# Kernel tuning notes

Measured on AMD Instinct MI355X. Metric: run time of the kernel, lower is better.

Reference implementation:

```python
import jax, jax.numpy as jnp
import numpy as np

H = 8        # heads
DH = 64      # dim_head
EPS = 1e-5   # LayerNorm eps (torch default)


def setup_inputs() -> dict:
    key = jax.random.key(0)
    k0, k1, k2, k3, k4 = jax.random.split(key, 5)
    b, l, n, dim = 2, 8, 256, 512
    inner = H * DH
    return {
        "xyzs": jax.random.normal(k0, (b, l, n, 3), dtype=jnp.float32),
        "features": jax.random.normal(k1, (b, l, n, dim), dtype=jnp.float32),
        "ln_gamma": jnp.ones((dim,), dtype=jnp.float32),
        "ln_beta": jnp.zeros((dim,), dtype=jnp.float32),
        "w_qkv": jax.random.normal(k2, (dim, 3 * inner), dtype=jnp.float32) * 0.02,
        "w_sp": jax.random.normal(k3, (3, DH), dtype=jnp.float32) * 0.3,
        "w_out": jax.random.normal(k4, (inner, dim), dtype=jnp.float32) * 0.02,
        "b_out": jnp.zeros((dim,), dtype=jnp.float32),
    }


def reference(xyzs, features, ln_gamma, ln_beta, w_qkv, w_sp, w_out, b_out):
    b, l, n, dim = features.shape
    m = l * n
    inner = H * DH
    scale = DH ** (-0.5)

    # LayerNorm over last dim (biased variance, eps=1e-5)
    mu = jnp.mean(features, axis=-1, keepdims=True)
    var = jnp.var(features, axis=-1, keepdims=True)
    normed = (features - mu) * jax.lax.rsqrt(var + EPS) * ln_gamma + ln_beta

    # qkv projection, chunk into q,k,v, reshape 'b l n (h d) -> b h (l n) d'
    qkv = normed.reshape(b, m, dim) @ w_qkv            # [b, m, 3*inner]
    def split_heads(t):
        return t.reshape(b, m, H, DH).transpose(0, 2, 1, 3)  # [b, h, m, d]
    q = split_heads(qkv[..., :inner])
    k = split_heads(qkv[..., inner:2 * inner])
    v = split_heads(qkv[..., 2 * inner:])

    dots = jnp.einsum('bhid,bhjd->bhij', q, k) * scale  # [b, h, m, m]
    attn = jax.nn.softmax(dots, axis=-1)
    v_out = jnp.einsum('bhij,bhjd->bhid', attn, v)      # [b, h, m, d]

    # pairwise coordinate deltas: delta[b,i,j,c] = xyz[b,j,c] - xyz[b,i,c]
    xyz_f = xyzs.reshape(b, m, 3)
    delta = xyz_f[:, None, :, :] - xyz_f[:, :, None, :]  # [b, m, m, 3]
    # attention-weighted aggregation over j (avoids [b,h,m,m,3] intermediate)
    agg = jnp.einsum('bhij,bijc->bhic', attn, delta)     # [b, h, m, 3]
    disp = agg @ w_sp                                    # [b, h, m, DH]

    out = v_out + disp                                   # [b, h, m, DH]
    out = out.transpose(0, 2, 1, 3).reshape(b, m, inner) # 'b h m d -> b m (h d)'
    out = jax.nn.gelu(out @ w_out + b_out, approximate=False)
    return out.reshape(b, l, n, dim) + features
```

## Files before the change

kernel.cpp:

```cpp
#include <hip/hip_runtime.h>
#include <hip/hip_bf16.h>
#include <math.h>

#define BB   2
#define MM   2048
#define DIM  512
#define NH   8
#define DHd  64
#define NQK  1536
#define ROWS 4096
#define NROW 32768
#define SPLITK 4

typedef __hip_bfloat16 bf16;
typedef __attribute__((ext_vector_type(8))) short bf16x8;
typedef __attribute__((ext_vector_type(4))) float f32x4;
typedef __attribute__((ext_vector_type(8))) unsigned short us8;

__device__ __forceinline__ unsigned short f2bf_bits(float x) {
    bf16 h = __float2bfloat16(x);
    return *(unsigned short*)&h;
}
__device__ __forceinline__ float bf2f(unsigned short u) {
    unsigned int v = ((unsigned int)u) << 16;
    return __uint_as_float(v);
}

__global__ __launch_bounds__(256) void pre_kernel(
    const float* __restrict__ feat, const float* __restrict__ gamma,
    const float* __restrict__ beta, unsigned short* __restrict__ normed,
    const float* __restrict__ wqkv, const float* __restrict__ wout,
    unsigned short* __restrict__ wqkvT, unsigned short* __restrict__ woutT)
{
    __shared__ float st[64][65];
    int b = blockIdx.x;
    int tid = threadIdx.x;
    if (b < ROWS) {
        const float* fr = feat + (size_t)b * DIM;
        float x0 = fr[tid];
        float x1 = fr[tid + 256];
        float s  = x0 + x1;
        float ss = x0 * x0 + x1 * x1;
        #pragma unroll
        for (int o = 32; o >= 1; o >>= 1) { s += __shfl_down(s, o); ss += __shfl_down(ss, o); }
        __shared__ float ws_[4], wss_[4];
        int wid = tid >> 6, lane = tid & 63;
        if (lane == 0) { ws_[wid] = s; wss_[wid] = ss; }
        __syncthreads();
        if (tid == 0) {
            float a = 0.f, c = 0.f;
            for (int i = 0; i < 4; i++) { a += ws_[i]; c += wss_[i]; }
            ws_[0] = a; wss_[0] = c;
        }
        __syncthreads();
        float mu  = ws_[0] * (1.0f / DIM);
        float var = wss_[0] * (1.0f / DIM) - mu * mu;
        float inv = rsqrtf(var + 1e-5f);
        normed[(size_t)b * DIM + tid]       = f2bf_bits((x0 - mu) * inv * gamma[tid] + beta[tid]);
        normed[(size_t)b * DIM + tid + 256] = f2bf_bits((x1 - mu) * inv * gamma[tid + 256] + beta[tid + 256]);
        return;
    }
    int idx = b - ROWS;
    const float* in; unsigned short* out; int N, n0;
    if (idx < 192) { in = wqkv; out = wqkvT; N = NQK; n0 = (idx >> 3) * 64; }
    else { idx -= 192; in = wout; out = woutT; N = DIM; n0 = (idx >> 3) * 64; }
    int k0 = (idx & 7) * 64;
    #pragma unroll
    for (int p = 0; p < 16; p++) {
        int e = tid + p * 256;
        int r = e >> 6, c = e & 63;
        st[r][c] = in[(size_t)(k0 + r) * N + n0 + c];
    }
    __syncthreads();
    #pragma unroll
    for (int p = 0; p < 16; p++) {
        int e = tid + p * 256;
        int nr = e >> 6, kc = e & 63;
        out[(size_t)(n0 + nr) * DIM + k0 + kc] = f2bf_bits(st[kc][nr]);
    }
}

__global__ __launch_bounds__(256) void qkv_gemm(
    const unsigned short* __restrict__ A, const unsigned short* __restrict__ BT,
    unsigned short* __restrict__ qd, unsigned short* __restrict__ kd,
    unsigned short* __restrict__ vd)
{
    __shared__ __align__(16) unsigned short sA[128 * 40];
    __shared__ __align__(16) unsigned short sB[128 * 40];
    int tid = threadIdx.x;
    int r0 = blockIdx.x * 128;
    int n0 = blockIdx.y * 128;
    int chunk = n0 >> 9;
    int cl    = n0 & 511;
    int w = tid >> 6, lane = tid & 63;
    int wm = w >> 1, wn = w & 1;
    int ln15 = lane & 15, quad = lane >> 4;

    int srow = tid >> 1;
    int scol = (tid & 1) * 16;

    f32x4 acc[4][4] = {};

    for (int k0 = 0; k0 < DIM; k0 += 32) {
        __syncthreads();
        *(us8*)&sA[srow * 40 + scol]     = *(const us8*)&A[(size_t)(r0 + srow) * DIM + k0 + scol];
        *(us8*)&sA[srow * 40 + scol + 8] = *(const us8*)&A[(size_t)(r0 + srow) * DIM + k0 + scol + 8];
        *(us8*)&sB[srow * 40 + scol]     = *(const us8*)&BT[(size_t)(n0 + srow) * DIM + k0 + scol];
        *(us8*)&sB[srow * 40 + scol + 8] = *(const us8*)&BT[(size_t)(n0 + srow) * DIM + k0 + scol + 8];
        __syncthreads();
        const unsigned short* fa = (chunk == 2) ? sA : sB;
        const unsigned short* fb = (chunk == 2) ? sB : sA;
        bf16x8 af[4], bf_[4];
        #pragma unroll
        for (int i = 0; i < 4; i++)
            af[i] = *(const bf16x8*)&fa[(wm * 64 + i * 16 + ln15) * 40 + quad * 8];
        #pragma unroll
        for (int j = 0; j < 4; j++)
            bf_[j] = *(const bf16x8*)&fb[(wn * 64 + j * 16 + ln15) * 40 + quad * 8];
        #pragma unroll
        for (int i = 0; i < 4; i++)
            #pragma unroll
            for (int j = 0; j < 4; j++)
                acc[i][j] = __builtin_amdgcn_mfma_f32_16x16x32_bf16(af[i], bf_[j], acc[i][j], 0, 0, 0);
    }

    if (chunk == 2) {
        int rowb = r0 + wm * 64 + quad * 4;
        #pragma unroll
        for (int j = 0; j < 4; j++) {
            int c = cl + wn * 64 + j * 16 + ln15;
            int h = c >> 6, d = c & 63;
            #pragma unroll
            for (int i = 0; i < 4; i++) {
                int gr = rowb + i * 16;
                int bb = gr >> 11, mm = gr & 2047;
                ushort4 pk;
                pk.x = f2bf_bits(acc[i][j][0]);
                pk.y = f2bf_bits(acc[i][j][1]);
                pk.z = f2bf_bits(acc[i][j][2]);
                pk.w = f2bf_bits(acc[i][j][3]);
                *(ushort4*)&vd[((size_t)(bb * NH + h) * DHd + d) * MM + mm] = pk;
            }
        }
    } else {
        unsigned short* dst = (chunk == 0) ? qd : kd;
        float sc = (chunk == 0) ? 0.125f : 1.0f;
        #pragma unroll
        for (int i = 0; i < 4; i++) {
            int within0 = cl + wm * 64 + i * 16 + quad * 4;
            int h = within0 >> 6, d = within0 & 63;
            #pragma unroll
            for (int j = 0; j < 4; j++) {
                int gr = r0 + wn * 64 + j * 16 + ln15;
                int bb = gr >> 11, mm = gr & 2047;
                ushort4 pk;
                pk.x = f2bf_bits(acc[i][j][0] * sc);
                pk.y = f2bf_bits(acc[i][j][1] * sc);
                pk.z = f2bf_bits(acc[i][j][2] * sc);
                pk.w = f2bf_bits(acc[i][j][3] * sc);
                *(ushort4*)&dst[((size_t)(bb * NH + h) * MM + mm) * DHd + d] = pk;
            }
        }
    }
}

__global__ __launch_bounds__(256, 4) void attn_kernel(
    const unsigned short* __restrict__ qg, const unsigned short* __restrict__ kg,
    const unsigned short* __restrict__ vg, const float* __restrict__ xyzs,
    unsigned short* __restrict__ obuf, float* __restrict__ lbuf)
{
    __shared__ __align__(16) unsigned short sK[64 * 72];
    __shared__ __align__(16) unsigned short sVT[80 * 72];
    __shared__ __align__(16) unsigned short sP[128 * 72];

    int tid = threadIdx.x;
    int bh = blockIdx.y; int bb = bh >> 3;
    int i0 = blockIdx.x * 128;
    int ks = blockIdx.z;
    int w = tid >> 6;
    int lane = tid & 63;
    int ln15 = lane & 15;
    int quad = lane >> 4;

    for (int e = tid; e < 12 * 72; e += 256) sVT[68 * 72 + e] = 0;
    if (tid < 64) sVT[67 * 72 + tid] = 0x3F80;

    bf16x8 aq[2][2];
    {
        const unsigned short* q0 = qg + ((size_t)bh * MM + i0 + w * 32 + ln15) * DHd + quad * 8;
        aq[0][0] = *(const bf16x8*)q0;
        aq[0][1] = *(const bf16x8*)(q0 + 32);
        aq[1][0] = *(const bf16x8*)(q0 + 16 * DHd);
        aq[1][1] = *(const bf16x8*)(q0 + 16 * DHd + 32);
    }

    f32x4 o[2][5] = {};

    const unsigned short* kbase = kg + (size_t)bh * MM * DHd;
    const unsigned short* vbase = vg + (size_t)bh * DHd * MM;
    int jbeg = ks * (MM / SPLITK), jend = jbeg + (MM / SPLITK);

    int srow = tid >> 2, scol16 = (tid & 3) * 16;

    us8 rk0, rk1, rv0, rv1;
    float rx = 0.f;
    {
        const unsigned short* src = kbase + (size_t)jbeg * DHd;
        rk0 = *(const us8*)&src[(size_t)tid * 16];
        rk1 = *(const us8*)&src[(size_t)tid * 16 + 8];
        const unsigned short* vs = vbase + jbeg;
        rv0 = *(const us8*)&vs[(size_t)srow * MM + scol16];
        rv1 = *(const us8*)&vs[(size_t)srow * MM + scol16 + 8];
        if (tid < 192) rx = xyzs[((size_t)bb * MM + jbeg) * 3 + tid];
    }

    int pwb = quad << 4;
    int swzr = (ln15 >> 2) << 4;
    int pr0 = (quad * 8) ^ swzr;
    int pr1 = (32 + quad * 8) ^ swzr;

    for (int jt = jbeg; jt < jend; jt += 64) {
        __syncthreads();
        *(us8*)&sK[srow * 72 + scol16]      = rk0;
        *(us8*)&sK[srow * 72 + scol16 + 8]  = rk1;
        *(us8*)&sVT[srow * 72 + scol16]     = rv0;
        *(us8*)&sVT[srow * 72 + scol16 + 8] = rv1;
        if (tid < 192) {
            int key = tid / 3, c = tid - key * 3;
            sVT[(64 + c) * 72 + key] = f2bf_bits(rx);
        }
        __syncthreads();
        int jn = jt + 64;
        if (jn < jend) {
            const unsigned short* src = kbase + (size_t)jn * DHd;
            rk0 = *(const us8*)&src[(size_t)tid * 16];
            rk1 = *(const us8*)&src[(size_t)tid * 16 + 8];
            const unsigned short* vs = vbase + jn;
            rv0 = *(const us8*)&vs[(size_t)srow * MM + scol16];
            rv1 = *(const us8*)&vs[(size_t)srow * MM + scol16 + 8];
            if (tid < 192) rx = xyzs[((size_t)bb * MM + jn) * 3 + tid];
        }

        #pragma unroll
        for (int t = 0; t < 4; t++) {
            bf16x8 bk0 = *(const bf16x8*)&sK[(t * 16 + ln15) * 72 + quad * 8];
            bf16x8 bk1 = *(const bf16x8*)&sK[(t * 16 + ln15) * 72 + 32 + quad * 8];
            int colb = (t * 16) ^ pwb;
            #pragma unroll
            for (int rf = 0; rf < 2; rf++) {
                f32x4 z = {};
                z = __builtin_amdgcn_mfma_f32_16x16x32_bf16(aq[rf][0], bk0, z, 0, 0, 0);
                z = __builtin_amdgcn_mfma_f32_16x16x32_bf16(aq[rf][1], bk1, z, 0, 0, 0);
                int rbase = (w * 32 + rf * 16 + quad * 4) * 72 + colb + ln15;
                sP[rbase]           = f2bf_bits(__expf(z[0]));
                sP[rbase + 72]      = f2bf_bits(__expf(z[1]));
                sP[rbase + 144]     = f2bf_bits(__expf(z[2]));
                sP[rbase + 216]     = f2bf_bits(__expf(z[3]));
            }
        }
        asm volatile("s_waitcnt lgkmcnt(0)" ::: "memory");
        bf16x8 ap[2][2];
        ap[0][0] = *(const bf16x8*)&sP[(w * 32 + ln15) * 72 + pr0];
        ap[0][1] = *(const bf16x8*)&sP[(w * 32 + ln15) * 72 + pr1];
        ap[1][0] = *(const bf16x8*)&sP[(w * 32 + 16 + ln15) * 72 + pr0];
        ap[1][1] = *(const bf16x8*)&sP[(w * 32 + 16 + ln15) * 72 + pr1];
        #pragma unroll
        for (int t = 0; t < 5; t++) {
            bf16x8 bv0 = *(const bf16x8*)&sVT[(t * 16 + ln15) * 72 + quad * 8];
            bf16x8 bv1 = *(const bf16x8*)&sVT[(t * 16 + ln15) * 72 + 32 + quad * 8];
            #pragma unroll
            for (int rf = 0; rf < 2; rf++) {
                o[rf][t] = __builtin_amdgcn_mfma_f32_16x16x32_bf16(ap[rf][0], bv0, o[rf][t], 0, 0, 0);
                o[rf][t] = __builtin_amdgcn_mfma_f32_16x16x32_bf16(ap[rf][1], bv1, o[rf][t], 0, 0, 0);
            }
        }
    }

    size_t kso = (size_t)ks * NROW;
    #pragma unroll
    for (int rf = 0; rf < 2; rf++) {
        #pragma unroll
        for (int reg = 0; reg < 4; reg++) {
            size_t row = (size_t)bh * MM + i0 + w * 32 + rf * 16 + quad * 4 + reg;
            unsigned short* orow = obuf + (kso + row) * 72;
            #pragma unroll
            for (int t = 0; t < 4; t++)
                orow[t * 16 + ln15] = f2bf_bits(o[rf][t][reg]);
            if (ln15 < 3)  orow[64 + ln15] = f2bf_bits(o[rf][4][reg]);
            if (ln15 == 3) lbuf[kso + row] = o[rf][4][reg];
        }
    }
}

__global__ __launch_bounds__(256) void merge_kernel(
    const unsigned short* __restrict__ obuf, const float* __restrict__ lbuf,
    const float* __restrict__ xyzs, const float* __restrict__ wsp,
    unsigned short* __restrict__ attn_out)
{
    __shared__ float sW[3][64];
    int tid = threadIdx.x;
    if (tid < 192) sW[tid >> 6][tid & 63] = wsp[tid];
    __syncthreads();
    int r   = blockIdx.x * 64 + (tid >> 2);
    int d0  = (tid & 3) * 16;
    int bh = r >> 11, qrow = r & 2047, bb = bh >> 3, hh = bh & 7;
    const unsigned short* p0 = obuf + (size_t)r * 72;
    const unsigned short* p1 = p0 + (size_t)NROW * 72;
    const unsigned short* p2 = p1 + (size_t)NROW * 72;
    const unsigned short* p3 = p2 + (size_t)NROW * 72;
    float invl = 1.f / (lbuf[r] + lbuf[NROW + r] + lbuf[2 * NROW + r] + lbuf[3 * NROW + r]);
    size_t xb = ((size_t)bb * MM + qrow) * 3;
    float gx = (bf2f(p0[64]) + bf2f(p1[64]) + bf2f(p2[64]) + bf2f(p3[64])) * invl - xyzs[xb + 0];
    float gy = (bf2f(p0[65]) + bf2f(p1[65]) + bf2f(p2[65]) + bf2f(p3[65])) * invl - xyzs[xb + 1];
    float gz = (bf2f(p0[66]) + bf2f(p1[66]) + bf2f(p2[66]) + bf2f(p3[66])) * invl - xyzs[xb + 2];
    us8 a0 = *(const us8*)&p0[d0];
    us8 a1 = *(const us8*)&p0[d0 + 8];
    us8 b0 = *(const us8*)&p1[d0];
    us8 b1 = *(const us8*)&p1[d0 + 8];
    us8 c0 = *(const us8*)&p2[d0];
    us8 c1 = *(const us8*)&p2[d0 + 8];
    us8 e0 = *(const us8*)&p3[d0];
    us8 e1 = *(const us8*)&p3[d0 + 8];
    unsigned short outv[16];
    #pragma unroll
    for (int e = 0; e < 8; e++) {
        int d = d0 + e;
        float v = (bf2f(a0[e]) + bf2f(b0[e]) + bf2f(c0[e]) + bf2f(e0[e])) * invl
                + gx * sW[0][d] + gy * sW[1][d] + gz * sW[2][d];
        outv[e] = f2bf_bits(v);
    }
    #pragma unroll
    for (int e = 0; e < 8; e++) {
        int d = d0 + 8 + e;
        float v = (bf2f(a1[e]) + bf2f(b1[e]) + bf2f(c1[e]) + bf2f(e1[e])) * invl
                + gx * sW[0][d] + gy * sW[1][d] + gz * sW[2][d];
        outv[8 + e] = f2bf_bits(v);
    }
    unsigned short* dst = attn_out + ((size_t)bb * MM + qrow) * DIM + hh * DHd + d0;
    *(us8*)dst       = *(us8*)&outv[0];
    *(us8*)(dst + 8) = *(us8*)&outv[8];
}

__global__ __launch_bounds__(256) void out_gemm(
    const unsigned short* __restrict__ A, const unsigned short* __restrict__ BT,
    const float* __restrict__ bias, const float* __restrict__ feat,
    float* __restrict__ out)
{
    __shared__ __align__(16) unsigned short sA[64 * 40];
    __shared__ __align__(16) unsigned short sB[64 * 40];
    int tid = threadIdx.x;
    int r0 = blockIdx.x * 64, n0 = blockIdx.y * 64;
    int w = tid >> 6, lane = tid & 63;
    int wm = w >> 1, wn = w & 1;
    int ln15 = lane & 15, quad = lane >> 4;

    int srow = tid >> 2, scol = (tid & 3) * 8;

    f32x4 acc[2][2] = {};

    for (int k0 = 0; k0 < DIM; k0 += 32) {
        __syncthreads();
        *(us8*)&sA[srow * 40 + scol] = *(const us8*)&A[(size_t)(r0 + srow) * DIM + k0 + scol];
        *(us8*)&sB[srow * 40 + scol] = *(const us8*)&BT[(size_t)(n0 + srow) * DIM + k0 + scol];
        __syncthreads();
        bf16x8 af[2], bf_[2];
        #pragma unroll
        for (int i = 0; i < 2; i++)
            af[i] = *(const bf16x8*)&sA[(wm * 32 + i * 16 + ln15) * 40 + quad * 8];
        #pragma unroll
        for (int j = 0; j < 2; j++)
            bf_[j] = *(const bf16x8*)&sB[(wn * 32 + j * 16 + ln15) * 40 + quad * 8];
        #pragma unroll
        for (int i = 0; i < 2; i++)
            #pragma unroll
            for (int j = 0; j < 2; j++)
                acc[i][j] = __builtin_amdgcn_mfma_f32_16x16x32_bf16(af[i], bf_[j], acc[i][j], 0, 0, 0);
    }

    #pragma unroll
    for (int i = 0; i < 2; i++) {
        #pragma unroll
        for (int reg = 0; reg < 4; reg++) {
            int gr = r0 + wm * 32 + i * 16 + quad * 4 + reg;
            #pragma unroll
            for (int j = 0; j < 2; j++) {
                int c = n0 + wn * 32 + j * 16 + ln15;
                float x = acc[i][j][reg] + bias[c];
                float g = 0.5f * x * (1.f + erff(x * 0.70710678118f));
                out[(size_t)gr * DIM + c] = g + feat[(size_t)gr * DIM + c];
            }
        }
    }
}

extern "C" void kernel_launch(void* const* d_in, const int* in_sizes, int n_in,
                              void* d_out, int out_size, void* d_ws, size_t ws_size,
                              hipStream_t stream)
{
    const float* xyzs  = (const float*)d_in[0];
    const float* feat  = (const float*)d_in[1];
    const float* gamma = (const float*)d_in[2];
    const float* beta  = (const float*)d_in[3];
    const float* wqkv  = (const float*)d_in[4];
    const float* wsp   = (const float*)d_in[5];
    const float* wout  = (const float*)d_in[6];
    const float* bout  = (const float*)d_in[7];
    float* out = (float*)d_out;

    unsigned short* ws16 = (unsigned short*)d_ws;
    const size_t SEGS = (size_t)ROWS * DIM;
    unsigned short* normed = ws16;
    unsigned short* qb     = ws16 + SEGS;
    unsigned short* kb     = ws16 + 2 * SEGS;
    unsigned short* vb     = ws16 + 3 * SEGS;
    unsigned short* wqkvT  = ws16 + 4 * SEGS;
    unsigned short* woutT  = wqkvT + (size_t)NQK * DIM;
    unsigned short* obuf   = woutT + (size_t)DIM * DIM;
    float*          lbuf   = (float*)(obuf + (size_t)SPLITK * NROW * 72);

    pre_kernel<<<ROWS + 256, 256, 0, stream>>>(feat, gamma, beta, normed,
                                               wqkv, wout, wqkvT, woutT);
    qkv_gemm<<<dim3(32, 12), 256, 0, stream>>>(normed, wqkvT, qb, kb, vb);
    attn_kernel<<<dim3(16, 16, SPLITK), 256, 0, stream>>>(qb, kb, vb, xyzs, obuf, lbuf);
    merge_kernel<<<512, 256, 0, stream>>>(obuf, lbuf, xyzs, wsp, normed);
    out_gemm<<<dim3(64, 8), 256, 0, stream>>>(normed, woutT, bout, feat, out);
}
```

Baseline: 150.1 us.

## Register-prefetch GEMM k-tiles, narrow QKV tiles, warp-per-row LayerNorm

```diff
diff --git a/kernel.cpp b/kernel.cpp
--- a/kernel.cpp
+++ b/kernel.cpp
@@ -35,32 +35,37 @@
     __shared__ float st[64][65];
     int b = blockIdx.x;
     int tid = threadIdx.x;
-    if (b < ROWS) {
-        const float* fr = feat + (size_t)b * DIM;
-        float x0 = fr[tid];
-        float x1 = fr[tid + 256];
-        float s  = x0 + x1;
-        float ss = x0 * x0 + x1 * x1;
-        #pragma unroll
-        for (int o = 32; o >= 1; o >>= 1) { s += __shfl_down(s, o); ss += __shfl_down(ss, o); }
-        __shared__ float ws_[4], wss_[4];
-        int wid = tid >> 6, lane = tid & 63;
-        if (lane == 0) { ws_[wid] = s; wss_[wid] = ss; }
-        __syncthreads();
-        if (tid == 0) {
-            float a = 0.f, c = 0.f;
-            for (int i = 0; i < 4; i++) { a += ws_[i]; c += wss_[i]; }
-            ws_[0] = a; wss_[0] = c;
-        }
-        __syncthreads();
-        float mu  = ws_[0] * (1.0f / DIM);
-        float var = wss_[0] * (1.0f / DIM) - mu * mu;
+    if (b < ROWS / 4) {
+        int w = tid >> 6, lane = tid & 63;
+        int row = b * 4 + w;
+        const float* fr = feat + (size_t)row * DIM + lane * 8;
+        float4 v0 = *(const float4*)fr;
+        float4 v1 = *(const float4*)(fr + 4);
+        float s  = v0.x + v0.y + v0.z + v0.w + v1.x + v1.y + v1.z + v1.w;
+        float ss = v0.x*v0.x + v0.y*v0.y + v0.z*v0.z + v0.w*v0.w
+                 + v1.x*v1.x + v1.y*v1.y + v1.z*v1.z + v1.w*v1.w;
+        #pragma unroll
+        for (int o = 32; o >= 1; o >>= 1) { s += __shfl_xor(s, o); ss += __shfl_xor(ss, o); }
+        float mu  = s * (1.0f / DIM);
+        float var = ss * (1.0f / DIM) - mu * mu;
         float inv = rsqrtf(var + 1e-5f);
-        normed[(size_t)b * DIM + tid]       = f2bf_bits((x0 - mu) * inv * gamma[tid] + beta[tid]);
-        normed[(size_t)b * DIM + tid + 256] = f2bf_bits((x1 - mu) * inv * gamma[tid + 256] + beta[tid + 256]);
+        const float* gp = gamma + lane * 8;
+        const float* bp = beta  + lane * 8;
+        float4 g0 = *(const float4*)gp, g1 = *(const float4*)(gp + 4);
+        float4 e0 = *(const float4*)bp, e1 = *(const float4*)(bp + 4);
+        unsigned short ov[8];
+        ov[0] = f2bf_bits((v0.x - mu) * inv * g0.x + e0.x);
+        ov[1] = f2bf_bits((v0.y - mu) * inv * g0.y + e0.y);
+        ov[2] = f2bf_bits((v0.z - mu) * inv * g0.z + e0.z);
+        ov[3] = f2bf_bits((v0.w - mu) * inv * g0.w + e0.w);
+        ov[4] = f2bf_bits((v1.x - mu) * inv * g1.x + e1.x);
+        ov[5] = f2bf_bits((v1.y - mu) * inv * g1.y + e1.y);
+        ov[6] = f2bf_bits((v1.z - mu) * inv * g1.z + e1.z);
+        ov[7] = f2bf_bits((v1.w - mu) * inv * g1.w + e1.w);
+        *(us8*)&normed[(size_t)row * DIM + lane * 8] = *(us8*)ov;
         return;
     }
-    int idx = b - ROWS;
+    int idx = b - ROWS / 4;
     const float* in; unsigned short* out; int N, n0;
     if (idx < 192) { in = wqkv; out = wqkvT; N = NQK; n0 = (idx >> 3) * 64; }
     else { idx -= 192; in = wout; out = woutT; N = DIM; n0 = (idx >> 3) * 64; }
@@ -85,55 +90,84 @@
     unsigned short* __restrict__ qd, unsigned short* __restrict__ kd,
     unsigned short* __restrict__ vd)
 {
-    __shared__ __align__(16) unsigned short sA[128 * 40];
-    __shared__ __align__(16) unsigned short sB[128 * 40];
+    __shared__ __align__(16) unsigned short sA[128 * 72];
+    __shared__ __align__(16) unsigned short sB[64 * 72];
     int tid = threadIdx.x;
     int r0 = blockIdx.x * 128;
-    int n0 = blockIdx.y * 128;
+    int n0 = blockIdx.y * 64;
     int chunk = n0 >> 9;
-    int cl    = n0 & 511;
+    int h     = (n0 & 511) >> 6;
     int w = tid >> 6, lane = tid & 63;
     int wm = w >> 1, wn = w & 1;
     int ln15 = lane & 15, quad = lane >> 4;
 
-    int srow = tid >> 1;
-    int scol = (tid & 1) * 16;
-
-    f32x4 acc[4][4] = {};
-
-    for (int k0 = 0; k0 < DIM; k0 += 32) {
-        __syncthreads();
-        *(us8*)&sA[srow * 40 + scol]     = *(const us8*)&A[(size_t)(r0 + srow) * DIM + k0 + scol];
-        *(us8*)&sA[srow * 40 + scol + 8] = *(const us8*)&A[(size_t)(r0 + srow) * DIM + k0 + scol + 8];
-        *(us8*)&sB[srow * 40 + scol]     = *(const us8*)&BT[(size_t)(n0 + srow) * DIM + k0 + scol];
-        *(us8*)&sB[srow * 40 + scol + 8] = *(const us8*)&BT[(size_t)(n0 + srow) * DIM + k0 + scol + 8];
-        __syncthreads();
-        const unsigned short* fa = (chunk == 2) ? sA : sB;
-        const unsigned short* fb = (chunk == 2) ? sB : sA;
-        bf16x8 af[4], bf_[4];
+    int arow = tid >> 1, acol = (tid & 1) * 32;
+    int brow = tid >> 2, bcol = (tid & 3) * 16;
+
+    f32x4 acc[4][2] = {};
+    us8 ra[4], rb[2];
+
+    #pragma unroll
+    for (int u = 0; u < 4; u++)
+        ra[u] = *(const us8*)&A[(size_t)(r0 + arow) * DIM + acol + u * 8];
+    #pragma unroll
+    for (int u = 0; u < 2; u++)
+        rb[u] = *(const us8*)&BT[(size_t)(n0 + brow) * DIM + bcol + u * 8];
+
+    for (int k0 = 0; k0 < DIM; k0 += 64) {
+        __syncthreads();
+        #pragma unroll
+        for (int u = 0; u < 4; u++) *(us8*)&sA[arow * 72 + acol + u * 8] = ra[u];
+        #pragma unroll
+        for (int u = 0; u < 2; u++) *(us8*)&sB[brow * 72 + bcol + u * 8] = rb[u];
+        __syncthreads();
+        int kn = k0 + 64;
+        if (kn < DIM) {
+            #pragma unroll
+            for (int u = 0; u < 4; u++)
+                ra[u] = *(const us8*)&A[(size_t)(r0 + arow) * DIM + kn + acol + u * 8];
+            #pragma unroll
+            for (int u = 0; u < 2; u++)
+                rb[u] = *(const us8*)&BT[(size_t)(n0 + brow) * DIM + kn + bcol + u * 8];
+        }
+        bf16x8 fa[4][2], fb[2][2];
         #pragma unroll
         for (int i = 0; i < 4; i++)
-            af[i] = *(const bf16x8*)&fa[(wm * 64 + i * 16 + ln15) * 40 + quad * 8];
-        #pragma unroll
-        for (int j = 0; j < 4; j++)
-            bf_[j] = *(const bf16x8*)&fb[(wn * 64 + j * 16 + ln15) * 40 + quad * 8];
-        #pragma unroll
-        for (int i = 0; i < 4; i++)
-            #pragma unroll
-            for (int j = 0; j < 4; j++)
-                acc[i][j] = __builtin_amdgcn_mfma_f32_16x16x32_bf16(af[i], bf_[j], acc[i][j], 0, 0, 0);
+            #pragma unroll
+            for (int kk = 0; kk < 2; kk++)
+                fa[i][kk] = *(const bf16x8*)&sA[(wm * 64 + i * 16 + ln15) * 72 + kk * 32 + quad * 8];
+        #pragma unroll
+        for (int j = 0; j < 2; j++)
+            #pragma unroll
+            for (int kk = 0; kk < 2; kk++)
+                fb[j][kk] = *(const bf16x8*)&sB[(wn * 32 + j * 16 + ln15) * 72 + kk * 32 + quad * 8];
+        if (chunk == 2) {
+            #pragma unroll
+            for (int kk = 0; kk < 2; kk++)
+                #pragma unroll
+                for (int i = 0; i < 4; i++)
+                    #pragma unroll
+                    for (int j = 0; j < 2; j++)
+                        acc[i][j] = __builtin_amdgcn_mfma_f32_16x16x32_bf16(fa[i][kk], fb[j][kk], acc[i][j], 0, 0, 0);
+        } else {
+            #pragma unroll
+            for (int kk = 0; kk < 2; kk++)
+                #pragma unroll
+                for (int i = 0; i < 4; i++)
+                    #pragma unroll
+                    for (int j = 0; j < 2; j++)
+                        acc[i][j] = __builtin_amdgcn_mfma_f32_16x16x32_bf16(fb[j][kk], fa[i][kk], acc[i][j], 0, 0, 0);
+        }
     }
 
     if (chunk == 2) {
-        int rowb = r0 + wm * 64 + quad * 4;
-        #pragma unroll
-        for (int j = 0; j < 4; j++) {
-            int c = cl + wn * 64 + j * 16 + ln15;
-            int h = c >> 6, d = c & 63;
-            #pragma unroll
-            for (int i = 0; i < 4; i++) {
-                int gr = rowb + i * 16;
-                int bb = gr >> 11, mm = gr & 2047;
+        #pragma unroll
+        for (int i = 0; i < 4; i++) {
+            int gm = r0 + wm * 64 + i * 16 + quad * 4;
+            int bb = gm >> 11, mm = gm & 2047;
+            #pragma unroll
+            for (int j = 0; j < 2; j++) {
+                int d = wn * 32 + j * 16 + ln15;
                 ushort4 pk;
                 pk.x = f2bf_bits(acc[i][j][0]);
                 pk.y = f2bf_bits(acc[i][j][1]);
@@ -147,18 +181,17 @@
         float sc = (chunk == 0) ? 0.125f : 1.0f;
         #pragma unroll
         for (int i = 0; i < 4; i++) {
-            int within0 = cl + wm * 64 + i * 16 + quad * 4;
-            int h = within0 >> 6, d = within0 & 63;
-            #pragma unroll
-            for (int j = 0; j < 4; j++) {
-                int gr = r0 + wn * 64 + j * 16 + ln15;
-                int bb = gr >> 11, mm = gr & 2047;
+            int gm = r0 + wm * 64 + i * 16 + ln15;
+            int bb = gm >> 11, mm = gm & 2047;
+            #pragma unroll
+            for (int j = 0; j < 2; j++) {
+                int d0 = wn * 32 + j * 16 + quad * 4;
                 ushort4 pk;
                 pk.x = f2bf_bits(acc[i][j][0] * sc);
                 pk.y = f2bf_bits(acc[i][j][1] * sc);
                 pk.z = f2bf_bits(acc[i][j][2] * sc);
                 pk.w = f2bf_bits(acc[i][j][3] * sc);
-                *(ushort4*)&dst[((size_t)(bb * NH + h) * MM + mm) * DHd + d] = pk;
+                *(ushort4*)&dst[((size_t)(bb * NH + h) * MM + mm) * DHd + d0] = pk;
             }
         }
     }
@@ -346,35 +379,59 @@
     const float* __restrict__ bias, const float* __restrict__ feat,
     float* __restrict__ out)
 {
-    __shared__ __align__(16) unsigned short sA[64 * 40];
-    __shared__ __align__(16) unsigned short sB[64 * 40];
+    __shared__ __align__(16) unsigned short sA[64 * 72];
+    __shared__ __align__(16) unsigned short sB[64 * 72];
     int tid = threadIdx.x;
     int r0 = blockIdx.x * 64, n0 = blockIdx.y * 64;
     int w = tid >> 6, lane = tid & 63;
     int wm = w >> 1, wn = w & 1;
     int ln15 = lane & 15, quad = lane >> 4;
 
-    int srow = tid >> 2, scol = (tid & 3) * 8;
+    int srow = tid >> 2, scol = (tid & 3) * 16;
 
     f32x4 acc[2][2] = {};
-
-    for (int k0 = 0; k0 < DIM; k0 += 32) {
-        __syncthreads();
-        *(us8*)&sA[srow * 40 + scol] = *(const us8*)&A[(size_t)(r0 + srow) * DIM + k0 + scol];
-        *(us8*)&sB[srow * 40 + scol] = *(const us8*)&BT[(size_t)(n0 + srow) * DIM + k0 + scol];
-        __syncthreads();
-        bf16x8 af[2], bf_[2];
+    us8 ra[2], rb[2];
+
+    #pragma unroll
+    for (int u = 0; u < 2; u++) {
+        ra[u] = *(const us8*)&A[(size_t)(r0 + srow) * DIM + scol + u * 8];
+        rb[u] = *(const us8*)&BT[(size_t)(n0 + srow) * DIM + scol + u * 8];
+    }
+
+    for (int k0 = 0; k0 < DIM; k0 += 64) {
+        __syncthreads();
+        #pragma unroll
+        for (int u = 0; u < 2; u++) {
+            *(us8*)&sA[srow * 72 + scol + u * 8] = ra[u];
+            *(us8*)&sB[srow * 72 + scol + u * 8] = rb[u];
+        }
+        __syncthreads();
+        int kn = k0 + 64;
+        if (kn < DIM) {
+            #pragma unroll
+            for (int u = 0; u < 2; u++) {
+                ra[u] = *(const us8*)&A[(size_t)(r0 + srow) * DIM + kn + scol + u * 8];
+                rb[u] = *(const us8*)&BT[(size_t)(n0 + srow) * DIM + kn + scol + u * 8];
+            }
+        }
+        bf16x8 af[2][2], bf_[2][2];
         #pragma unroll
         for (int i = 0; i < 2; i++)
-            af[i] = *(const bf16x8*)&sA[(wm * 32 + i * 16 + ln15) * 40 + quad * 8];
+            #pragma unroll
+            for (int kk = 0; kk < 2; kk++)
+                af[i][kk] = *(const bf16x8*)&sA[(wm * 32 + i * 16 + ln15) * 72 + kk * 32 + quad * 8];
         #pragma unroll
         for (int j = 0; j < 2; j++)
-            bf_[j] = *(const bf16x8*)&sB[(wn * 32 + j * 16 + ln15) * 40 + quad * 8];
-        #pragma unroll
-        for (int i = 0; i < 2; i++)
-            #pragma unroll
-            for (int j = 0; j < 2; j++)
-                acc[i][j] = __builtin_amdgcn_mfma_f32_16x16x32_bf16(af[i], bf_[j], acc[i][j], 0, 0, 0);
+            #pragma unroll
+            for (int kk = 0; kk < 2; kk++)
+                bf_[j][kk] = *(const bf16x8*)&sB[(wn * 32 + j * 16 + ln15) * 72 + kk * 32 + quad * 8];
+        #pragma unroll
+        for (int kk = 0; kk < 2; kk++)
+            #pragma unroll
+            for (int i = 0; i < 2; i++)
+                #pragma unroll
+                for (int j = 0; j < 2; j++)
+                    acc[i][j] = __builtin_amdgcn_mfma_f32_16x16x32_bf16(af[i][kk], bf_[j][kk], acc[i][j], 0, 0, 0);
     }
 
     #pragma unroll
@@ -418,9 +475,9 @@
     unsigned short* obuf   = woutT + (size_t)DIM * DIM;
     float*          lbuf   = (float*)(obuf + (size_t)SPLITK * NROW * 72);
 
-    pre_kernel<<<ROWS + 256, 256, 0, stream>>>(feat, gamma, beta, normed,
-                                               wqkv, wout, wqkvT, woutT);
-    qkv_gemm<<<dim3(32, 12), 256, 0, stream>>>(normed, wqkvT, qb, kb, vb);
+    pre_kernel<<<ROWS / 4 + 256, 256, 0, stream>>>(feat, gamma, beta, normed,
+                                                   wqkv, wout, wqkvT, woutT);
+    qkv_gemm<<<dim3(32, 24), 256, 0, stream>>>(normed, wqkvT, qb, kb, vb);
     attn_kernel<<<dim3(16, 16, SPLITK), 256, 0, stream>>>(qb, kb, vb, xyzs, obuf, lbuf);
     merge_kernel<<<512, 256, 0, stream>>>(obuf, lbuf, xyzs, wsp, normed);
     out_gemm<<<dim3(64, 8), 256, 0, stream>>>(normed, woutT, bout, feat, out);
```

Measured after the change: 144.1 us. 3.9% less time.
